# Optimization experiments

Hardware: AMD Instinct MI355X
Metric: run time of the kernel (lower is better)

## Reference

```python
import jax, jax.numpy as jnp
import numpy as np

K = 7          # kernel_size
PAD = K // 2   # padding


def _unfold(t):
    """im2col for kxk neighborhood: (B,C,H,W) -> (B,C,K*K,H,W), zero-padded."""
    B, C, H, W = t.shape
    p = jnp.pad(t, ((0, 0), (0, 0), (PAD, PAD), (PAD, PAD)))
    # row-major over kernel offsets matches F.unfold ordering
    wins = jnp.stack([p[:, :, i:i + H, j:j + W]
                      for i in range(K) for j in range(K)], axis=2)
    return wins


def setup_inputs() -> dict:
    key = jax.random.key(0)
    ks = jax.random.split(key, 7)
    B, C, H, W = 8, 128, 64, 64
    scale = 1.0 / np.sqrt(C)
    x = jax.random.normal(ks[0], (B, C, H, W), dtype=jnp.float32)
    Wq = jax.random.normal(ks[1], (C, C), dtype=jnp.float32) * scale
    Wk = jax.random.normal(ks[2], (C, C), dtype=jnp.float32) * scale
    Wv = jax.random.normal(ks[3], (C, C), dtype=jnp.float32) * scale
    bq = jax.random.normal(ks[4], (C,), dtype=jnp.float32) * 0.01
    bk = jax.random.normal(ks[5], (C,), dtype=jnp.float32) * 0.01
    bv = jax.random.normal(ks[6], (C,), dtype=jnp.float32) * 0.01
    return {"x": x, "Wq": Wq, "bq": bq, "Wk": Wk, "bk": bk, "Wv": Wv, "bv": bv}


def reference(x, Wq, bq, Wk, bk, Wv, bv):
    # 1x1 convs = channel GEMMs
    q = jnp.einsum('oc,bchw->bohw', Wq, x) + bq[:, None, None]
    k = jnp.einsum('oc,bchw->bohw', Wk, x) + bk[:, None, None]
    v = jnp.einsum('oc,bchw->bohw', Wv, x) + bv[:, None, None]
    k_unf = _unfold(k)   # (B,C,K*K,H,W)
    v_unf = _unfold(v)   # (B,C,K*K,H,W)
    # attention scores over the K*K neighborhood, summed over channels
    attn = jnp.einsum('bchw,bcphw->bphw', q, k_unf)
    attn = jax.nn.softmax(attn, axis=1)
    y = jnp.einsum('bphw,bcphw->bchw', attn, v_unf)
    return y
```

## Files before the change

### kernel.cpp

```cpp
#include <hip/hip_runtime.h>
#include <hip/hip_bf16.h>

#define CC   128
#define HH_  64
#define WW_  64
#define BB   8
#define HWSZ (HH_*WW_)
#define CHW  (CC*HWSZ)
#define BCHW (BB*CHW)
#define PAD  3
#define NP   49

typedef __attribute__((ext_vector_type(8))) short short8;
typedef __attribute__((ext_vector_type(4))) float float4v;

__global__ __launch_bounds__(256) void prep_w(
    const float* __restrict__ Wq, const float* __restrict__ Wk,
    const float* __restrict__ Wv,
    unsigned short* __restrict__ whi, unsigned short* __restrict__ wlo)
{
    int i = blockIdx.x * 256 + threadIdx.x;
    const float* src = (i < 16384) ? Wq : (i < 32768 ? Wk : Wv);
    float f = src[i & 16383];
    __hip_bfloat16 h = __float2bfloat16(f);
    float hf = __bfloat162float(h);
    __hip_bfloat16 l = __float2bfloat16(f - hf);
    unsigned short hu, lu;
    __builtin_memcpy(&hu, &h, 2);
    __builtin_memcpy(&lu, &l, 2);
    whi[i] = hu;
    wlo[i] = lu;
}

__global__ __launch_bounds__(256, 2) void qkv_mfma(
    const float* __restrict__ x,
    const unsigned short* __restrict__ whi, const unsigned short* __restrict__ wlo,
    const float* __restrict__ bq, const float* __restrict__ bk,
    const float* __restrict__ bv, float* __restrict__ qkv)
{
    __shared__ unsigned short xT[2][128][136];
    const int proj = blockIdx.y;
    const int n0g  = blockIdx.x << 7;
    const int b    = n0g >> 12;
    const int npx  = n0g & 4095;
    const int tid  = threadIdx.x;
    const int lane = tid & 63;
    const int wv   = tid >> 6;
    const int wm   = wv & 1, wn = wv >> 1;

    const float* xb = x + (size_t)b*CHW + npx;
    #pragma unroll
    for (int it = 0; it < 16; ++it) {
        int f  = tid + (it << 8);
        int c  = f >> 5;
        int p4 = (f & 31) << 2;
        float4 v = *(const float4*)&xb[(size_t)c*HWSZ + p4];
        float vv[4] = {v.x, v.y, v.z, v.w};
        #pragma unroll
        for (int u = 0; u < 4; ++u) {
            __hip_bfloat16 h = __float2bfloat16(vv[u]);
            float hf = __bfloat162float(h);
            __hip_bfloat16 l = __float2bfloat16(vv[u] - hf);
            unsigned short hu, lu;
            __builtin_memcpy(&hu, &h, 2);
            __builtin_memcpy(&lu, &l, 2);
            xT[0][p4 + u][c] = hu;
            xT[1][p4 + u][c] = lu;
        }
    }

    const float* Bp = (proj == 0) ? bq : (proj == 1 ? bk : bv);
    const int q4 = lane >> 4;
    float4v acc[4][4];
    #pragma unroll
    for (int sm = 0; sm < 4; ++sm) {
        const int mb = wm*64 + sm*16 + q4*4;
        float4v bi;
        bi[0] = Bp[mb+0]; bi[1] = Bp[mb+1]; bi[2] = Bp[mb+2]; bi[3] = Bp[mb+3];
        #pragma unroll
        for (int sn = 0; sn < 4; ++sn) acc[sm][sn] = bi;
    }

    __syncthreads();

    const unsigned short* Wh = whi + (size_t)proj*16384;
    const unsigned short* Wl = wlo + (size_t)proj*16384;
    const int kq8  = q4 << 3;
    const int mrow = lane & 15;

    for (int pass = 0; pass < 3; ++pass) {
        const unsigned short* Wp = (pass == 2) ? Wl : Wh;
        const int xi = (pass == 1) ? 1 : 0;
        #pragma unroll
        for (int kc = 0; kc < 4; ++kc) {
            const int kb = kc << 5;
            short8 a[4], bf[4];
            #pragma unroll
            for (int sm = 0; sm < 4; ++sm) {
                const int m = wm*64 + sm*16 + mrow;
                a[sm] = *(const short8*)&Wp[(size_t)m*CC + kb + kq8];
            }
            #pragma unroll
            for (int sn = 0; sn < 4; ++sn) {
                const int n = wn*64 + sn*16 + mrow;
                bf[sn] = *(const short8*)&xT[xi][n][kb + kq8];
            }
            #pragma unroll
            for (int sm = 0; sm < 4; ++sm)
                #pragma unroll
                for (int sn = 0; sn < 4; ++sn)
                    acc[sm][sn] = __builtin_amdgcn_mfma_f32_16x16x32_bf16(
                        a[sm], bf[sn], acc[sm][sn], 0, 0, 0);
        }
    }

    float* op = qkv + (size_t)proj*BCHW + (size_t)b*CHW + npx;
    #pragma unroll
    for (int sm = 0; sm < 4; ++sm) {
        const int mb = wm*64 + sm*16 + q4*4;
        #pragma unroll
        for (int sn = 0; sn < 4; ++sn) {
            const int n = wn*64 + sn*16 + mrow;
            #pragma unroll
            for (int r = 0; r < 4; ++r)
                op[(size_t)(mb + r)*HWSZ + n] = acc[sm][sn][r];
        }
    }
}

__device__ __forceinline__ void load_chunk8(const float* __restrict__ src,
                                            int h0, int c0, float4* stg) {
    const int tid = threadIdx.x;
    #pragma unroll
    for (int i = 0; i < 4; ++i) {
        int f   = tid + (i << 9);
        int c   = f >> 7;
        int rem = f & 127;
        int r   = rem >> 4;
        int q4  = (rem & 15) << 2;
        int hh  = h0 - PAD + r;
        if ((unsigned)hh < (unsigned)HH_)
            stg[i] = *(const float4*)&src[(size_t)(c0 + c)*HWSZ + hh*WW_ + q4];
        else
            stg[i] = make_float4(0.f, 0.f, 0.f, 0.f);
    }
}

__device__ __forceinline__ void store_chunk8(float (*ks)[8][72], const float4* stg) {
    const int tid = threadIdx.x;
    #pragma unroll
    for (int i = 0; i < 4; ++i) {
        int f   = tid + (i << 9);
        int c   = f >> 7;
        int rem = f & 127;
        int r   = rem >> 4;
        int q4  = (rem & 15) << 2;
        *(float4*)&ks[c][r][4 + q4] = stg[i];
    }
}

__global__ __launch_bounds__(512) void locatt(
    const float* __restrict__ qkv, float* __restrict__ out)
{
    __shared__ float ks[16][8][72];
    __shared__ float lg[2][NP][64];
    __shared__ float dn[2][64];

    const int blk = blockIdx.x;
    const int x   = blk & 7;
    const int j   = blk >> 3;
    const int b   = j >> 2;
    const int h0  = (((x << 2) | (j & 3)) << 1);
    const int tid = threadIdx.x;
    const int s   = tid >> 6;
    const int w   = tid & 63;

    const float* qp = qkv + (size_t)b*CHW;
    const float* kp = qkv + (size_t)BCHW + (size_t)b*CHW;
    const float* vp = qkv + (size_t)2*BCHW + (size_t)b*CHW;

    if (tid < 256) {
        int idx = tid & 127;
        int c = idx >> 3, r = idx & 7;
        int col = (tid < 128) ? 0 : 68;
        *(float4*)&ks[c][r][col] = make_float4(0.f, 0.f, 0.f, 0.f);
    }

    const bool do0 = (s < 7);
    const bool do1 = (s >= 1);

    float acc0[7], acc1[7];
    #pragma unroll
    for (int dx = 0; dx < 7; ++dx) { acc0[dx] = 0.f; acc1[dx] = 0.f; }

    float4 stg[4];
    load_chunk8(kp, h0, 0, stg);

    for (int ck = 0; ck < 8; ++ck) {
        store_chunk8(ks, stg);
        __syncthreads();
        if (ck < 7) load_chunk8(kp, h0, (ck + 1) * 16, stg);

        const int c0 = ck << 4;
        float q0[16], q1[16];
        #pragma unroll
        for (int ci = 0; ci < 16; ++ci) {
            const float* qc = qp + (size_t)(c0 + ci)*HWSZ + h0*WW_ + w;
            q0[ci] = do0 ? qc[0]   : 0.f;
            q1[ci] = do1 ? qc[WW_] : 0.f;
        }

        const float* kbase = &ks[0][s][w + 1];
        #pragma unroll
        for (int ci = 0; ci < 16; ++ci) {
            const float* kc = kbase + ci * 576;
            #pragma unroll
            for (int dx = 0; dx < 7; ++dx) {
                float kv = kc[dx];
                acc0[dx] = fmaf(q0[ci], kv, acc0[dx]);
                acc1[dx] = fmaf(q1[ci], kv, acc1[dx]);
            }
        }
        __syncthreads();
    }

    #pragma unroll
    for (int dx = 0; dx < 7; ++dx) {
        if (do0) lg[0][s*7 + dx][w]     = acc0[dx];
        if (do1) lg[1][(s-1)*7 + dx][w] = acc1[dx];
    }
    load_chunk8(vp, h0, 0, stg);
    __syncthreads();

    if (tid < 128) {
        const int r = tid >> 6, px = tid & 63;
        float tv[NP];
        float m = -1e30f;
        #pragma unroll
        for (int p = 0; p < NP; ++p) { tv[p] = lg[r][p][px]; m = fmaxf(m, tv[p]); }
        float d = 0.f;
        #pragma unroll
        for (int p = 0; p < NP; ++p) {
            float e = __expf(tv[p] - m);
            d += e;
            lg[r][p][px] = e;
        }
        dn[r][px] = 1.f / d;
    }
    __syncthreads();

    float a0[NP], a1[NP];
    const float sc0 = dn[0][w], sc1 = dn[1][w];
    #pragma unroll
    for (int p = 0; p < NP; ++p) a0[p] = lg[0][p][w] * sc0;
    #pragma unroll
    for (int p = 0; p < NP; ++p) a1[p] = lg[1][p][w] * sc1;

    for (int ck = 0; ck < 8; ++ck) {
        store_chunk8(ks, stg);
        __syncthreads();
        if (ck < 7) load_chunk8(vp, h0, (ck + 1) * 16, stg);

        #pragma unroll
        for (int half = 0; half < 2; ++half) {
            const int cl = s + (half << 3);
            float y0 = 0.f, y1 = 0.f;
            #pragma unroll
            for (int r = 0; r < 8; ++r) {
                const float* vr = &ks[cl][r][w + 1];
                #pragma unroll
                for (int dx = 0; dx < 7; ++dx) {
                    float vv = vr[dx];
                    if (r < 7)  y0 = fmaf(a0[r*7 + dx], vv, y0);
                    if (r >= 1) y1 = fmaf(a1[(r-1)*7 + dx], vv, y1);
                }
            }
            float* op = out + (size_t)b*CHW + (size_t)(ck*16 + cl)*HWSZ
                            + (size_t)h0*WW_ + w;
            op[0]   = y0;
            op[WW_] = y1;
        }
        __syncthreads();
    }
}

extern "C" void kernel_launch(void* const* d_in, const int* in_sizes, int n_in,
                              void* d_out, int out_size, void* d_ws, size_t ws_size,
                              hipStream_t stream) {
    const float* x  = (const float*)d_in[0];
    const float* Wq = (const float*)d_in[1];
    const float* bq = (const float*)d_in[2];
    const float* Wk = (const float*)d_in[3];
    const float* bk = (const float*)d_in[4];
    const float* Wv = (const float*)d_in[5];
    const float* bv = (const float*)d_in[6];
    float* out = (float*)d_out;
    float* qkv = (float*)d_ws;

    unsigned short* whi = (unsigned short*)d_out;
    unsigned short* wlo = whi + 3*16384;

    prep_w  <<<192, 256, 0, stream>>>(Wq, Wk, Wv, whi, wlo);
    qkv_mfma<<<dim3(256, 3), 256, 0, stream>>>(x, whi, wlo, bq, bk, bv, qkv);
    locatt  <<<256, 512, 0, stream>>>(qkv, out);
}
```

Before: 144.6 us.

## Vectorize QK logits per lane and use transposed padded smem for V

In the QK phase, each lane now computes four adjacent output columns over a quarter of the channels, using float4 loads from smem and global memory. The partial sums are combined with cross-lane shuffles. In the AV phase, V is staged through registers into a channel-minor smem layout padded to 17 floats, so each thread reads two channels per load stride and accumulates two channels at once. The goal is to cut LDS instruction count and bank conflicts. The cost is higher register pressure from the 7x4x2 accumulators and extra shuffle reductions.

Result: no change. 144.4 us (-0.2%).

```diff
diff --git a/kernel.cpp b/kernel.cpp
--- a/kernel.cpp
+++ b/kernel.cpp
@@ -146,38 +146,31 @@
     }
 }
 
-__device__ __forceinline__ void store_chunk8(float (*ks)[8][72], const float4* stg) {
-    const int tid = threadIdx.x;
-    #pragma unroll
-    for (int i = 0; i < 4; ++i) {
-        int f   = tid + (i << 9);
-        int c   = f >> 7;
-        int rem = f & 127;
-        int r   = rem >> 4;
-        int q4  = (rem & 15) << 2;
-        *(float4*)&ks[c][r][4 + q4] = stg[i];
-    }
-}
-
 __global__ __launch_bounds__(512) void locatt(
     const float* __restrict__ qkv, float* __restrict__ out)
 {
-    __shared__ float ks[16][8][72];
+    __shared__ __align__(16) float smem[8*72*17];
     __shared__ float lg[2][NP][64];
     __shared__ float dn[2][64];
 
     const int blk = blockIdx.x;
-    const int x   = blk & 7;
-    const int j   = blk >> 3;
-    const int b   = j >> 2;
-    const int h0  = (((x << 2) | (j & 3)) << 1);
+    const int xs  = blk & 7;
+    const int jj  = blk >> 3;
+    const int b   = jj >> 2;
+    const int h0  = (((xs << 2) | (jj & 3)) << 1);
     const int tid = threadIdx.x;
     const int s   = tid >> 6;
-    const int w   = tid & 63;
+    const int lane = tid & 63;
+    const int q16  = lane & 15;
+    const int csub = lane >> 4;
+    const int w4   = q16 << 2;
+    const int w    = lane;
 
     const float* qp = qkv + (size_t)b*CHW;
     const float* kp = qkv + (size_t)BCHW + (size_t)b*CHW;
     const float* vp = qkv + (size_t)2*BCHW + (size_t)b*CHW;
+
+    float (*ks)[8][72] = (float(*)[8][72])smem;
 
     if (tid < 256) {
         int idx = tid & 127;
@@ -189,47 +182,86 @@
     const bool do0 = (s < 7);
     const bool do1 = (s >= 1);
 
-    float acc0[7], acc1[7];
-    #pragma unroll
-    for (int dx = 0; dx < 7; ++dx) { acc0[dx] = 0.f; acc1[dx] = 0.f; }
+    float acc0[7][4], acc1[7][4];
+    #pragma unroll
+    for (int dx = 0; dx < 7; ++dx)
+        #pragma unroll
+        for (int j = 0; j < 4; ++j) { acc0[dx][j] = 0.f; acc1[dx][j] = 0.f; }
 
     float4 stg[4];
     load_chunk8(kp, h0, 0, stg);
 
     for (int ck = 0; ck < 8; ++ck) {
-        store_chunk8(ks, stg);
+        #pragma unroll
+        for (int i = 0; i < 4; ++i) {
+            int f   = tid + (i << 9);
+            int c   = f >> 7;
+            int rem = f & 127;
+            int r   = rem >> 4;
+            int q4  = (rem & 15) << 2;
+            *(float4*)&ks[c][r][4 + q4] = stg[i];
+        }
         __syncthreads();
         if (ck < 7) load_chunk8(kp, h0, (ck + 1) * 16, stg);
 
         const int c0 = ck << 4;
-        float q0[16], q1[16];
-        #pragma unroll
-        for (int ci = 0; ci < 16; ++ci) {
-            const float* qc = qp + (size_t)(c0 + ci)*HWSZ + h0*WW_ + w;
-            q0[ci] = do0 ? qc[0]   : 0.f;
-            q1[ci] = do1 ? qc[WW_] : 0.f;
-        }
-
-        const float* kbase = &ks[0][s][w + 1];
-        #pragma unroll
-        for (int ci = 0; ci < 16; ++ci) {
-            const float* kc = kbase + ci * 576;
-            #pragma unroll
-            for (int dx = 0; dx < 7; ++dx) {
-                float kv = kc[dx];
-                acc0[dx] = fmaf(q0[ci], kv, acc0[dx]);
-                acc1[dx] = fmaf(q1[ci], kv, acc1[dx]);
-            }
+        #pragma unroll
+        for (int ci4 = 0; ci4 < 4; ++ci4) {
+            const int c = (ci4 << 2) + csub;
+            const float* qc = qp + (size_t)(c0 + c)*HWSZ + h0*WW_ + w4;
+            float4 q0v = do0 ? *(const float4*)qc
+                             : make_float4(0.f, 0.f, 0.f, 0.f);
+            float4 q1v = do1 ? *(const float4*)(qc + WW_)
+                             : make_float4(0.f, 0.f, 0.f, 0.f);
+            float4 ka  = *(const float4*)&ks[c][s][w4];
+            float4 kb  = *(const float4*)&ks[c][s][w4 + 4];
+            float4 kc2 = *(const float4*)&ks[c][s][w4 + 8];
+            float kw[12] = {ka.x,ka.y,ka.z,ka.w, kb.x,kb.y,kb.z,kb.w,
+                            kc2.x,kc2.y,kc2.z,kc2.w};
+            float q0a[4] = {q0v.x,q0v.y,q0v.z,q0v.w};
+            float q1a[4] = {q1v.x,q1v.y,q1v.z,q1v.w};
+            #pragma unroll
+            for (int dx = 0; dx < 7; ++dx)
+                #pragma unroll
+                for (int j = 0; j < 4; ++j) {
+                    float kv = kw[j + dx + 1];
+                    acc0[dx][j] = fmaf(q0a[j], kv, acc0[dx][j]);
+                    acc1[dx][j] = fmaf(q1a[j], kv, acc1[dx][j]);
+                }
         }
         __syncthreads();
     }
 
     #pragma unroll
+    for (int dx = 0; dx < 7; ++dx)
+        #pragma unroll
+        for (int j = 0; j < 4; ++j) {
+            acc0[dx][j] += __shfl_xor(acc0[dx][j], 16, 64);
+            acc0[dx][j] += __shfl_xor(acc0[dx][j], 32, 64);
+            acc1[dx][j] += __shfl_xor(acc1[dx][j], 16, 64);
+            acc1[dx][j] += __shfl_xor(acc1[dx][j], 32, 64);
+        }
+    #pragma unroll
     for (int dx = 0; dx < 7; ++dx) {
-        if (do0) lg[0][s*7 + dx][w]     = acc0[dx];
-        if (do1) lg[1][(s-1)*7 + dx][w] = acc1[dx];
-    }
-    load_chunk8(vp, h0, 0, stg);
+        if ((dx & 3) == csub) {
+            if (do0) *(float4*)&lg[0][s*7 + dx][w4] =
+                make_float4(acc0[dx][0], acc0[dx][1], acc0[dx][2], acc0[dx][3]);
+            if (do1) *(float4*)&lg[1][(s-1)*7 + dx][w4] =
+                make_float4(acc1[dx][0], acc1[dx][1], acc1[dx][2], acc1[dx][3]);
+        }
+    }
+
+    float vreg[16];
+    {
+        #pragma unroll
+        for (int i = 0; i < 16; ++i) {
+            int c  = 2*s + (i >> 3);
+            int r  = i & 7;
+            int hh = h0 - PAD + r;
+            vreg[i] = ((unsigned)hh < (unsigned)HH_)
+                      ? vp[(size_t)c*HWSZ + hh*WW_ + w] : 0.f;
+        }
+    }
     __syncthreads();
 
     if (tid < 128) {
@@ -246,6 +278,15 @@
             lg[r][p][px] = e;
         }
         dn[r][px] = 1.f / d;
+    } else {
+        int t = tid - 128;
+        for (int i = t; i < 1024; i += 384) {
+            int r    = i >> 7;
+            int rem  = i & 127;
+            int colg = rem >> 4;
+            int col  = (colg < 4) ? colg : (64 + colg);
+            smem[r*1224 + col*17 + (rem & 15)] = 0.f;
+        }
     }
     __syncthreads();
 
@@ -257,29 +298,48 @@
     for (int p = 0; p < NP; ++p) a1[p] = lg[1][p][w] * sc1;
 
     for (int ck = 0; ck < 8; ++ck) {
-        store_chunk8(ks, stg);
+        #pragma unroll
+        for (int i = 0; i < 16; ++i) {
+            int c = 2*s + (i >> 3);
+            int r = i & 7;
+            smem[r*1224 + (4 + w)*17 + c] = vreg[i];
+        }
         __syncthreads();
-        if (ck < 7) load_chunk8(vp, h0, (ck + 1) * 16, stg);
-
-        #pragma unroll
-        for (int half = 0; half < 2; ++half) {
-            const int cl = s + (half << 3);
-            float y0 = 0.f, y1 = 0.f;
-            #pragma unroll
-            for (int r = 0; r < 8; ++r) {
-                const float* vr = &ks[cl][r][w + 1];
-                #pragma unroll
-                for (int dx = 0; dx < 7; ++dx) {
-                    float vv = vr[dx];
-                    if (r < 7)  y0 = fmaf(a0[r*7 + dx], vv, y0);
-                    if (r >= 1) y1 = fmaf(a1[(r-1)*7 + dx], vv, y1);
+        if (ck < 7) {
+            int c0v = (ck + 1) << 4;
+            #pragma unroll
+            for (int i = 0; i < 16; ++i) {
+                int c  = 2*s + (i >> 3);
+                int r  = i & 7;
+                int hh = h0 - PAD + r;
+                vreg[i] = ((unsigned)hh < (unsigned)HH_)
+                          ? vp[(size_t)(c0v + c)*HWSZ + hh*WW_ + w] : 0.f;
+            }
+        }
+        float y0a = 0.f, y0b = 0.f, y1a = 0.f, y1b = 0.f;
+        #pragma unroll
+        for (int r = 0; r < 8; ++r) {
+            const float* vbase = &smem[r*1224 + (1 + w)*17 + 2*s];
+            #pragma unroll
+            for (int dx = 0; dx < 7; ++dx) {
+                float va = vbase[17*dx];
+                float vb = vbase[17*dx + 1];
+                if (r < 7) {
+                    float aw = a0[r*7 + dx];
+                    y0a = fmaf(aw, va, y0a); y0b = fmaf(aw, vb, y0b);
+                }
+                if (r >= 1) {
+                    float aw = a1[(r-1)*7 + dx];
+                    y1a = fmaf(aw, va, y1a); y1b = fmaf(aw, vb, y1b);
                 }
             }
-            float* op = out + (size_t)b*CHW + (size_t)(ck*16 + cl)*HWSZ
-                            + (size_t)h0*WW_ + w;
-            op[0]   = y0;
-            op[WW_] = y1;
-        }
+        }
+        float* op = out + (size_t)b*CHW + (size_t)(ck*16 + 2*s)*HWSZ
+                        + (size_t)h0*WW_ + w;
+        op[0]          = y0a;
+        op[WW_]        = y1a;
+        op[HWSZ]       = y0b;
+        op[HWSZ + WW_] = y1b;
         __syncthreads();
     }
 }
```
